# Optimization experiments

Measured on AMD Instinct MI355X. Metric: run time of the kernel, lower is better.

## Reference

```python
import jax, jax.numpy as jnp
import numpy as np

D_MODEL = 1024
NHEAD = 16
HEAD_DIM = D_MODEL // NHEAD
LN_EPS = 1e-5
ROPE_BASE = 10000.0


def _rope_cos_sin(n, head_dim):
    inv_freq = 1.0 / (ROPE_BASE ** (jnp.arange(0, head_dim, 2, dtype=jnp.float32) / head_dim))
    t = jnp.arange(n, dtype=jnp.float32)
    freqs = jnp.outer(t, inv_freq)  # (N, head_dim//2)
    return jnp.cos(freqs), jnp.sin(freqs)


def _apply_rope(x, cos, sin):
    # x: (B, H, N, hd); cos/sin: (N, hd//2)
    B, H, N, hd = x.shape
    xr = x.reshape(B, H, N, hd // 2, 2)
    x0, x1 = xr[..., 0], xr[..., 1]
    c = cos[None, None]
    s = sin[None, None]
    rot = jnp.stack([x0 * c - x1 * s, x0 * s + x1 * c], axis=-1)
    return rot.reshape(B, H, N, hd)


def setup_inputs() -> dict:
    key = jax.random.key(0)
    ks = jax.random.split(key, 6)
    D = D_MODEL
    scale = 1.0 / np.sqrt(D)
    x = jax.random.normal(ks[0], (2, 2048, D), dtype=jnp.float32)
    Wq = jax.random.normal(ks[1], (D, D), dtype=jnp.float32) * scale
    Wk = jax.random.normal(ks[2], (D, D), dtype=jnp.float32) * scale
    Wv = jax.random.normal(ks[3], (D, D), dtype=jnp.float32) * scale
    Wo = jax.random.normal(ks[4], (D, D), dtype=jnp.float32) * scale
    bq = jnp.zeros((D,), jnp.float32)
    bk = jnp.zeros((D,), jnp.float32)
    bv = jnp.zeros((D,), jnp.float32)
    bo = jnp.zeros((D,), jnp.float32)
    ln_w = jnp.ones((D,), jnp.float32)
    ln_b = jnp.zeros((D,), jnp.float32)
    return {"x": x, "ln_w": ln_w, "ln_b": ln_b, "Wq": Wq, "bq": bq,
            "Wk": Wk, "bk": bk, "Wv": Wv, "bv": bv, "Wo": Wo, "bo": bo}


def reference(x, ln_w, ln_b, Wq, bq, Wk, bk, Wv, bv, Wo, bo):
    B, N, D = x.shape
    H, hd = NHEAD, HEAD_DIM
    # LayerNorm
    mu = jnp.mean(x, axis=-1, keepdims=True)
    var = jnp.mean(jnp.square(x - mu), axis=-1, keepdims=True)
    xn = (x - mu) * jax.lax.rsqrt(var + LN_EPS) * ln_w + ln_b
    # QKV projections -> (B, H, N, hd)
    def proj(W, b):
        return (xn @ W.T + b).reshape(B, N, H, hd).transpose(0, 2, 1, 3)
    q = proj(Wq, bq)
    k = proj(Wk, bk)
    v = proj(Wv, bv)
    cos, sin = _rope_cos_sin(N, hd)
    q = _apply_rope(q, cos, sin)
    k = _apply_rope(k, cos, sin)
    scores = jnp.einsum('bhqd,bhkd->bhqk', q, k) / jnp.sqrt(jnp.float32(hd))
    attn = jax.nn.softmax(scores, axis=-1)
    out = jnp.einsum('bhqk,bhkd->bhqd', attn, v)
    out = out.transpose(0, 2, 1, 3).reshape(B, N, D)
    return x + out @ Wo.T + bo
```

## Files before the change

### kernel.cpp

```cpp
#include <hip/hip_runtime.h>


#define SEQ 2048
#define LN_EPS 1e-5f

using short8 = __attribute__((ext_vector_type(8))) short;
using f32x4  = __attribute__((ext_vector_type(4))) float;
using f32x16 = __attribute__((ext_vector_type(16))) float;

__device__ __forceinline__ unsigned short f2bf(float f) {
  union { float f; unsigned u; } v; v.f = f;
  unsigned r = v.u + 0x7FFFu + ((v.u >> 16) & 1u);
  return (unsigned short)(r >> 16);
}

__device__ __forceinline__ void async16(const void* g, void* l) {
  __builtin_amdgcn_global_load_lds(
      (const __attribute__((address_space(1))) void*)g,
      (__attribute__((address_space(3))) void*)l, 16, 0, 0);
}

__global__ __launch_bounds__(256) void prep_kernel(
    const float* __restrict__ x, const float* __restrict__ lnw, const float* __restrict__ lnb,
    const float* __restrict__ wq, const float* __restrict__ wk,
    const float* __restrict__ wv, const float* __restrict__ wo,
    unsigned short* __restrict__ wqkv, unsigned short* __restrict__ wob,
    unsigned short* __restrict__ xn, float2* __restrict__ tab) {
  const int b = blockIdx.x, t = threadIdx.x;
  if (b < 4096) {
    const int gid = b * 256 + t;
    const int m = gid >> 18, e4 = gid & 262143;
    const float* src = (m == 0) ? wq : (m == 1) ? wk : (m == 2) ? wv : wo;
    const float4 v = ((const float4*)src)[e4];
    ushort4 o; o.x = f2bf(v.x); o.y = f2bf(v.y); o.z = f2bf(v.z); o.w = f2bf(v.w);
    if (m < 3) ((ushort4*)wqkv)[(size_t)m * 262144 + e4] = o;
    else       ((ushort4*)wob)[e4] = o;
  } else if (b < 8192) {
    const int row = b - 4096;
    const float4 v = ((const float4*)(x + (size_t)row * 1024))[t];
    float s  = v.x + v.y + v.z + v.w;
    float s2 = v.x * v.x + v.y * v.y + v.z * v.z + v.w * v.w;
#pragma unroll
    for (int off = 32; off >= 1; off >>= 1) {
      s  += __shfl_xor(s, off);
      s2 += __shfl_xor(s2, off);
    }
    __shared__ float red[8];
    const int lane = t & 63, wave = t >> 6;
    if (lane == 0) { red[wave] = s; red[4 + wave] = s2; }
    __syncthreads();
    s  = red[0] + red[1] + red[2] + red[3];
    s2 = red[4] + red[5] + red[6] + red[7];
    const float mu   = s * (1.0f / 1024.0f);
    const float var  = s2 * (1.0f / 1024.0f) - mu * mu;
    const float rstd = rsqrtf(var + LN_EPS);
    const float4 wv4 = ((const float4*)lnw)[t];
    const float4 bv4 = ((const float4*)lnb)[t];
    ushort4 o;
    o.x = f2bf((v.x - mu) * rstd * wv4.x + bv4.x);
    o.y = f2bf((v.y - mu) * rstd * wv4.y + bv4.y);
    o.z = f2bf((v.z - mu) * rstd * wv4.z + bv4.z);
    o.w = f2bf((v.w - mu) * rstd * wv4.w + bv4.w);
    ((ushort4*)xn)[(size_t)row * 256 + t] = o;
  } else {
    const int gid = (b - 8192) * 256 + t;
    const int pos = gid >> 5, ip = gid & 31;
    const float invf = exp2f((float)ip * -0.4152410118609203f);
    const float fr = (float)pos * invf;
    tab[gid] = make_float2(cosf(fr), sinf(fr));
  }
}

__global__ __launch_bounds__(256, 3) void gemm_qkv_kernel(
    const unsigned short* __restrict__ A,
    const unsigned short* __restrict__ Bw,
    const float* __restrict__ bq, const float* __restrict__ bk, const float* __restrict__ bv,
    const float2* __restrict__ tab,
    unsigned short* __restrict__ qb, unsigned short* __restrict__ kbg,
    unsigned short* __restrict__ vtb) {
  __shared__ unsigned short lA[128 * 64];
  __shared__ unsigned short lB[128 * 64];
  const int tid = threadIdx.x;
  const int lane = tid & 63, wave = tid >> 6;
  const int lr = lane & 15, quad = lane >> 4;
  const int wm = (wave >> 1) * 64, wn = (wave & 1) * 64;
  const int n0 = blockIdx.x * 128, m0 = blockIdx.y * 128;
  const int r7 = lr & 7;
  const int lrow = lane >> 3, lcg = (lane & 7) ^ lrow;
  const int lin = blockIdx.y * gridDim.x + blockIdx.x;
  const int phase = ((lin >> 8) * 5) & 15;

  f32x4 acc[4][4];
#pragma unroll
  for (int i = 0; i < 4; ++i)
#pragma unroll
    for (int j = 0; j < 4; ++j) acc[i][j] = (f32x4){0.f, 0.f, 0.f, 0.f};

#define QKV_STAGE(kt_) {                                                        \
    const int kofs = (((kt_) + phase) & 15) * 64;                               \
    _Pragma("unroll")                                                           \
    for (int c = 0; c < 4; ++c) {                                               \
      const int chunk = wave * 4 + c;                                           \
      const int grow = chunk * 8 + lrow;                                        \
      async16(&A[(size_t)(m0 + grow) * 1024 + kofs + lcg * 8], &lA[chunk * 512]);\
      async16(&Bw[(size_t)(n0 + grow) * 1024 + kofs + lcg * 8], &lB[chunk * 512]);\
    }                                                                           \
  }

  QKV_STAGE(0);
  __syncthreads();

  for (int kt = 0; kt < 16; ++kt) {
    short8 a[2][4], b[2][4];
#pragma unroll
    for (int kk = 0; kk < 2; ++kk) {
#pragma unroll
      for (int i = 0; i < 4; ++i)
        a[kk][i] = *(const short8*)&lA[(wm + i * 16 + lr) * 64 + ((kk * 4 + quad) ^ r7) * 8];
#pragma unroll
      for (int j = 0; j < 4; ++j)
        b[kk][j] = *(const short8*)&lB[(wn + j * 16 + lr) * 64 + ((kk * 4 + quad) ^ r7) * 8];
    }
    __syncthreads();
    if (kt < 15) QKV_STAGE(kt + 1);
#pragma unroll
    for (int kk = 0; kk < 2; ++kk)
#pragma unroll
      for (int i = 0; i < 4; ++i)
#pragma unroll
        for (int j = 0; j < 4; ++j)
          acc[i][j] = __builtin_amdgcn_mfma_f32_16x16x32_bf16(a[kk][i], b[kk][j], acc[i][j], 0, 0, 0);
    __syncthreads();
  }

  const int which = n0 >> 10;
  const float* bias = (which == 0) ? bq : (which == 1) ? bk : bv;
  const float qs = (which == 0) ? 0.18033688011112042f : 1.0f;
#pragma unroll
  for (int i = 0; i < 4; ++i)
#pragma unroll
    for (int j = 0; j < 4; ++j)
#pragma unroll
      for (int r = 0; r < 4; ++r) {
        const int row = m0 + wm + i * 16 + quad * 4 + r;
        const int col = n0 + wn + j * 16 + lr;
        const int c = col & 1023;
        float val = (acc[i][j][r] + bias[c]) * qs;
        const int head = c >> 6, hd_i = c & 63;
        const int b_ = row >> 11, pos = row & 2047;
        if (which < 2) {
          const float partner = __shfl_xor(val, 1);
          const float2 cs = tab[(pos << 5) + (hd_i >> 1)];
          val = val * cs.x + partner * ((lane & 1) ? cs.y : -cs.y);
        }
        if (which == 2) {
          vtb[((size_t)((b_ * 16 + head) * 64 + hd_i)) * SEQ + pos] = f2bf(val);
        } else {
          const size_t didx = ((size_t)((b_ * 16 + head) * SEQ + pos)) * 64 + hd_i;
          if (which == 0) qb[didx] = f2bf(val);
          else            kbg[didx] = f2bf(val);
        }
      }
}

__global__ __launch_bounds__(256, 4) void gemm_o_kernel(
    const unsigned short* __restrict__ A,
    const unsigned short* __restrict__ Bw,
    const float* __restrict__ bo, const float* __restrict__ xres, float* __restrict__ out) {
  __shared__ unsigned short lA[64 * 64];
  __shared__ unsigned short lB[64 * 64];
  const int tid = threadIdx.x;
  const int lane = tid & 63, wave = tid >> 6;
  const int lr = lane & 15, quad = lane >> 4;
  const int wm = (wave >> 1) * 32, wn = (wave & 1) * 32;
  const int n0 = blockIdx.x * 64, m0 = blockIdx.y * 64;
  const int r7 = lr & 7;
  const int lrow = lane >> 3, lcg = (lane & 7) ^ lrow;
  const int lin = blockIdx.y * gridDim.x + blockIdx.x;
  const int phase = ((lin >> 8) * 4) & 15;

  f32x4 acc[2][2];
#pragma unroll
  for (int i = 0; i < 2; ++i)
#pragma unroll
    for (int j = 0; j < 2; ++j) acc[i][j] = (f32x4){0.f, 0.f, 0.f, 0.f};

#define O_STAGE(kt_) {                                                          \
    const int kofs = (((kt_) + phase) & 15) * 64;                               \
    _Pragma("unroll")                                                           \
    for (int c = 0; c < 2; ++c) {                                               \
      const int chunk = wave * 2 + c;                                           \
      const int grow = chunk * 8 + lrow;                                        \
      async16(&A[(size_t)(m0 + grow) * 1024 + kofs + lcg * 8], &lA[chunk * 512]);\
      async16(&Bw[(size_t)(n0 + grow) * 1024 + kofs + lcg * 8], &lB[chunk * 512]);\
    }                                                                           \
  }

  O_STAGE(0);
  __syncthreads();

  for (int kt = 0; kt < 16; ++kt) {
    short8 a[2][2], b[2][2];
#pragma unroll
    for (int kk = 0; kk < 2; ++kk) {
#pragma unroll
      for (int i = 0; i < 2; ++i)
        a[kk][i] = *(const short8*)&lA[(wm + i * 16 + lr) * 64 + ((kk * 4 + quad) ^ r7) * 8];
#pragma unroll
      for (int j = 0; j < 2; ++j)
        b[kk][j] = *(const short8*)&lB[(wn + j * 16 + lr) * 64 + ((kk * 4 + quad) ^ r7) * 8];
    }
    __syncthreads();
    if (kt < 15) O_STAGE(kt + 1);
#pragma unroll
    for (int kk = 0; kk < 2; ++kk)
#pragma unroll
      for (int i = 0; i < 2; ++i)
#pragma unroll
        for (int j = 0; j < 2; ++j)
          acc[i][j] = __builtin_amdgcn_mfma_f32_16x16x32_bf16(a[kk][i], b[kk][j], acc[i][j], 0, 0, 0);
    __syncthreads();
  }

#pragma unroll
  for (int i = 0; i < 2; ++i)
#pragma unroll
    for (int j = 0; j < 2; ++j)
#pragma unroll
      for (int r = 0; r < 4; ++r) {
        const int row = m0 + wm + i * 16 + quad * 4 + r;
        const int col = n0 + wn + j * 16 + lr;
        const size_t idx = (size_t)row * 1024 + col;
        out[idx] = acc[i][j][r] + bo[col] + xres[idx];
      }
}

__global__ __launch_bounds__(512, 4) void attn_kernel(
    const unsigned short* __restrict__ qg, const unsigned short* __restrict__ kg,
    const unsigned short* __restrict__ vtg, unsigned short* __restrict__ ao) {
  __shared__ unsigned short lds[32768];
  const int tid = threadIdx.x;
  const int lane = tid & 63, w = tid >> 6;
  const int ws = w & 3, kh = w >> 2;
  const int l31 = lane & 31, hb = lane >> 5;
  const int bh = blockIdx.x >> 4, qt = blockIdx.x & 15;
  const int q0w = qt * 128 + ws * 32;
  const int phase32 = ((blockIdx.x >> 8) & 1) * 16;
  const unsigned short* Q  = qg + (size_t)bh * SEQ * 64;
  const unsigned short* K  = kg + (size_t)bh * SEQ * 64;
  const unsigned short* VT = vtg + (size_t)bh * 64 * SEQ;

  short8 qf[4];
#pragma unroll
  for (int c = 0; c < 4; ++c)
    qf[c] = *(const short8*)&Q[(size_t)(q0w + l31) * 64 + c * 16 + hb * 8];

  f32x16 o[2];
#pragma unroll
  for (int dh = 0; dh < 2; ++dh)
#pragma unroll
    for (int r = 0; r < 16; ++r) o[dh][r] = 0.f;
  float ls = 0.f;

  const int khbase = kh * 1024;
  const int srow_k = ws * 8 + (lane >> 3), gk = lane & 7;
  const int srow_v = ws * 16 + (lane >> 2), gv = lane & 3;
  const unsigned short* Ksrc = K + (size_t)(khbase + srow_k) * 64 + gk * 8;
  const unsigned short* Vsrc = VT + (size_t)srow_v * SEQ + khbase + gv * 8;
  const int kds = (gk * 32 + (srow_k ^ gk)) * 8;
  const int g2s = gv * 2 + (srow_v >> 5);
  const int vds = (g2s * 32 + ((srow_v & 31) ^ g2s)) * 8;
  unsigned short* const base_kh = lds + kh * 4096;

  int koff[4], voff[2][2];
#pragma unroll
  for (int c = 0; c < 4; ++c) {
    const int fk = c * 2 + hb;
    koff[c] = (fk * 32 + (l31 ^ fk)) * 8;
  }
#pragma unroll
  for (int cl = 0; cl < 2; ++cl)
#pragma unroll
    for (int dh = 0; dh < 2; ++dh) {
      const int f = (cl * 2 + hb) * 2 + dh;
      voff[cl][dh] = 2048 + (f * 32 + (l31 ^ f)) * 8;
    }

  auto TILE = [&](const unsigned short* Tb) {
    f32x16 sv;
#pragma unroll
    for (int r = 0; r < 16; ++r) sv[r] = 0.f;
    __builtin_amdgcn_s_setprio(1);
#pragma unroll
    for (int c = 0; c < 4; ++c) {
      const short8 af = *(const short8*)&Tb[koff[c]];
      sv = __builtin_amdgcn_mfma_f32_32x32x16_bf16(af, qf[c], sv, 0, 0, 0);
    }
    __builtin_amdgcn_s_setprio(0);
    unsigned wp[8];
#pragma unroll
    for (int p = 0; p < 8; ++p) {
      union { float f; unsigned u; } e0, e1;
      e0.f = __builtin_amdgcn_exp2f(sv[2 * p]);
      e1.f = __builtin_amdgcn_exp2f(sv[2 * p + 1]);
      ls += e0.f + e1.f;
      wp[p] = __builtin_amdgcn_perm(e1.u, e0.u, 0x07060302u);
    }
    unsigned wlo[8], whi[8];
#pragma unroll
    for (int p = 0; p < 8; ++p) {
      auto rr = __builtin_amdgcn_permlane32_swap(wp[p], wp[p], false, false);
      wlo[p] = rr[0]; whi[p] = rr[1];
    }
    __builtin_amdgcn_s_setprio(1);
#pragma unroll
    for (int cl = 0; cl < 2; ++cl) {
      const int pb = cl * 4;
      union { unsigned u[4]; short8 s; } pf;
      pf.u[0] = hb ? wlo[pb + 2] : wlo[pb + 0];
      pf.u[1] = hb ? wlo[pb + 3] : wlo[pb + 1];
      pf.u[2] = hb ? whi[pb + 2] : whi[pb + 0];
      pf.u[3] = hb ? whi[pb + 3] : whi[pb + 1];
#pragma unroll
      for (int dh = 0; dh < 2; ++dh) {
        const short8 vf = *(const short8*)&Tb[voff[cl][dh]];
        o[dh] = __builtin_amdgcn_mfma_f32_32x32x16_bf16(pf.s, vf, o[dh], 0, 0, 0);
      }
    }
    __builtin_amdgcn_s_setprio(0);
  };

#pragma unroll
  for (int j = 0; j < 2; ++j) {
    const int tl = (j + phase32) & 31;
    const short8 R0 = *(const short8*)(Ksrc + (size_t)tl * 2048);
    const short8 R2 = *(const short8*)(Vsrc + tl * 32);
    *(short8*)(base_kh + j * 8192 + kds) = R0;
    *(short8*)(base_kh + j * 8192 + 2048 + vds) = R2;
  }
  __syncthreads();

  for (int it = 0; it < 16; ++it) {
    const int cs = (it & 1) * 2;
    const int ss = cs ^ 2;
    short8 R0, R2;
    if (it < 15) {
      const int tl = (2 * it + 2 + phase32) & 31;
      R0 = *(const short8*)(Ksrc + (size_t)tl * 2048);
      R2 = *(const short8*)(Vsrc + tl * 32);
    }
    TILE(base_kh + cs * 8192);
    if (it < 15) {
      *(short8*)(base_kh + ss * 8192 + kds) = R0;
      *(short8*)(base_kh + ss * 8192 + 2048 + vds) = R2;
      const int tl = (2 * it + 3 + phase32) & 31;
      R0 = *(const short8*)(Ksrc + (size_t)tl * 2048);
      R2 = *(const short8*)(Vsrc + tl * 32);
    }
    TILE(base_kh + (cs + 1) * 8192);
    if (it < 15) {
      *(short8*)(base_kh + (ss + 1) * 8192 + kds) = R0;
      *(short8*)(base_kh + (ss + 1) * 8192 + 2048 + vds) = R2;
    }
    __syncthreads();
  }

  union { float f; unsigned u; } lsu; lsu.f = ls;
  auto lr2 = __builtin_amdgcn_permlane32_swap(lsu.u, lsu.u, false, false);
  union { unsigned u; float f; } la, lb2; la.u = lr2[0]; lb2.u = lr2[1];
  const float lsH = la.f + lb2.f;

  float* osh = (float*)lds;
  float* lsh = (float*)(lds + 16384);
  if (kh == 1) {
#pragma unroll
    for (int dh = 0; dh < 2; ++dh)
#pragma unroll
      for (int r = 0; r < 16; ++r)
        osh[((ws * 2 + dh) * 16 + r) * 64 + lane] = o[dh][r];
    lsh[ws * 64 + lane] = lsH;
  }
  __syncthreads();
  if (kh == 0) {
    const float rl = 1.0f / (lsH + lsh[ws * 64 + lane]);
    const int b_ = bh >> 4, h = bh & 15;
#pragma unroll
    for (int r = 0; r < 16; ++r) {
      const int m = (r & 3) + 8 * (r >> 2) + 4 * hb;
      const float rlv = __shfl(rl, m);
      const int row = q0w + m;
#pragma unroll
      for (int dh = 0; dh < 2; ++dh) {
        const float ov = o[dh][r] + osh[((ws * 2 + dh) * 16 + r) * 64 + lane];
        ao[(size_t)(b_ * SEQ + row) * 1024 + h * 64 + dh * 32 + l31] = f2bf(ov * rlv);
      }
    }
  }
}

extern "C" void kernel_launch(void* const* d_in, const int* in_sizes, int n_in,
                              void* d_out, int out_size, void* d_ws, size_t ws_size,
                              hipStream_t stream) {
  const float* x   = (const float*)d_in[0];
  const float* lnw = (const float*)d_in[1];
  const float* lnb = (const float*)d_in[2];
  const float* Wq  = (const float*)d_in[3];
  const float* bq  = (const float*)d_in[4];
  const float* Wk  = (const float*)d_in[5];
  const float* bk  = (const float*)d_in[6];
  const float* Wv  = (const float*)d_in[7];
  const float* bv  = (const float*)d_in[8];
  const float* Wo  = (const float*)d_in[9];
  const float* bo  = (const float*)d_in[10];
  float* out = (float*)d_out;

  char* ws = (char*)d_ws;
  unsigned short* wqkv = (unsigned short*)(ws);
  unsigned short* wob  = (unsigned short*)(ws + 6291456);
  unsigned short* xn   = (unsigned short*)(ws + 8388608);
  unsigned short* qb   = (unsigned short*)(ws + 16777216);
  unsigned short* kbuf = (unsigned short*)(ws + 25165824);
  unsigned short* vtb  = (unsigned short*)(ws + 33554432);
  unsigned short* ao   = (unsigned short*)(ws + 41943040);
  float2*         tab  = (float2*)(ws + 50331648);

  hipLaunchKernelGGL(prep_kernel, dim3(8448), dim3(256), 0, stream,
                     x, lnw, lnb, Wq, Wk, Wv, Wo, wqkv, wob, xn, tab);
  hipLaunchKernelGGL(gemm_qkv_kernel, dim3(24, 32), dim3(256), 0, stream,
                     xn, wqkv, bq, bk, bv, tab, qb, kbuf, vtb);
  hipLaunchKernelGGL(attn_kernel, dim3(512), dim3(512), 0, stream, qb, kbuf, vtb, ao);
  hipLaunchKernelGGL(gemm_o_kernel, dim3(16, 64), dim3(256), 0, stream,
                     ao, wob, bo, x, out);
}
```

Baseline: 208.0 us.

## Double-buffer QKV GEMM LDS tiles and remap blocks for XCD-aware locality

Result: slower. 229.2 us (+10.2%).

```diff
diff --git a/kernel.cpp b/kernel.cpp
--- a/kernel.cpp
+++ b/kernel.cpp
@@ -71,23 +71,26 @@
   }
 }
 
-__global__ __launch_bounds__(256, 3) void gemm_qkv_kernel(
+__global__ __launch_bounds__(256, 2) void gemm_qkv_kernel(
     const unsigned short* __restrict__ A,
     const unsigned short* __restrict__ Bw,
     const float* __restrict__ bq, const float* __restrict__ bk, const float* __restrict__ bv,
     const float2* __restrict__ tab,
     unsigned short* __restrict__ qb, unsigned short* __restrict__ kbg,
     unsigned short* __restrict__ vtb) {
-  __shared__ unsigned short lA[128 * 64];
-  __shared__ unsigned short lB[128 * 64];
+  __shared__ unsigned short lA[2][128 * 64];
+  __shared__ unsigned short lB[2][128 * 64];
   const int tid = threadIdx.x;
   const int lane = tid & 63, wave = tid >> 6;
   const int lr = lane & 15, quad = lane >> 4;
   const int wm = (wave >> 1) * 64, wn = (wave & 1) * 64;
-  const int n0 = blockIdx.x * 128, m0 = blockIdx.y * 128;
+  const int lin = blockIdx.x;
+  const int rg = lin & 7, q = lin >> 3;
+  const int bx = (rg & 1) * 12 + q % 12;
+  const int by = (rg >> 1) * 8 + q / 12;
+  const int n0 = bx * 128, m0 = by * 128;
   const int r7 = lr & 7;
   const int lrow = lane >> 3, lcg = (lane & 7) ^ lrow;
-  const int lin = blockIdx.y * gridDim.x + blockIdx.x;
   const int phase = ((lin >> 8) * 5) & 15;
 
   f32x4 acc[4][4];
@@ -96,33 +99,40 @@
 #pragma unroll
     for (int j = 0; j < 4; ++j) acc[i][j] = (f32x4){0.f, 0.f, 0.f, 0.f};
 
-#define QKV_STAGE(kt_) {                                                        \
+#define QKV_STAGE(kt_, LA_, LB_) {                                              \
     const int kofs = (((kt_) + phase) & 15) * 64;                               \
     _Pragma("unroll")                                                           \
     for (int c = 0; c < 4; ++c) {                                               \
       const int chunk = wave * 4 + c;                                           \
       const int grow = chunk * 8 + lrow;                                        \
-      async16(&A[(size_t)(m0 + grow) * 1024 + kofs + lcg * 8], &lA[chunk * 512]);\
-      async16(&Bw[(size_t)(n0 + grow) * 1024 + kofs + lcg * 8], &lB[chunk * 512]);\
+      async16(&A[(size_t)(m0 + grow) * 1024 + kofs + lcg * 8], &(LA_)[chunk * 512]); \
+      async16(&Bw[(size_t)(n0 + grow) * 1024 + kofs + lcg * 8], &(LB_)[chunk * 512]); \
     }                                                                           \
   }
 
-  QKV_STAGE(0);
-  __syncthreads();
+  QKV_STAGE(0, lA[0], lB[0]);
+  QKV_STAGE(1, lA[1], lB[1]);
+  asm volatile("s_waitcnt vmcnt(8)" ::: "memory");
+  __builtin_amdgcn_sched_barrier(0);
+  __builtin_amdgcn_s_barrier();
 
   for (int kt = 0; kt < 16; ++kt) {
+    const int cur = kt & 1;
     short8 a[2][4], b[2][4];
 #pragma unroll
     for (int kk = 0; kk < 2; ++kk) {
 #pragma unroll
       for (int i = 0; i < 4; ++i)
-        a[kk][i] = *(const short8*)&lA[(wm + i * 16 + lr) * 64 + ((kk * 4 + quad) ^ r7) * 8];
+        a[kk][i] = *(const short8*)&lA[cur][(wm + i * 16 + lr) * 64 + ((kk * 4 + quad) ^ r7) * 8];
 #pragma unroll
       for (int j = 0; j < 4; ++j)
-        b[kk][j] = *(const short8*)&lB[(wn + j * 16 + lr) * 64 + ((kk * 4 + quad) ^ r7) * 8];
-    }
-    __syncthreads();
-    if (kt < 15) QKV_STAGE(kt + 1);
+        b[kk][j] = *(const short8*)&lB[cur][(wn + j * 16 + lr) * 64 + ((kk * 4 + quad) ^ r7) * 8];
+    }
+    asm volatile("s_waitcnt lgkmcnt(0)" ::: "memory");
+    __builtin_amdgcn_sched_barrier(0);
+    __builtin_amdgcn_s_barrier();
+    __builtin_amdgcn_sched_barrier(0);
+    if (kt < 14) QKV_STAGE(kt + 2, lA[cur], lB[cur]);
 #pragma unroll
     for (int kk = 0; kk < 2; ++kk)
 #pragma unroll
@@ -130,7 +140,13 @@
 #pragma unroll
         for (int j = 0; j < 4; ++j)
           acc[i][j] = __builtin_amdgcn_mfma_f32_16x16x32_bf16(a[kk][i], b[kk][j], acc[i][j], 0, 0, 0);
-    __syncthreads();
+    if (kt < 15) {
+      if (kt < 14) asm volatile("s_waitcnt vmcnt(8)" ::: "memory");
+      else         asm volatile("s_waitcnt vmcnt(0)" ::: "memory");
+      __builtin_amdgcn_sched_barrier(0);
+      __builtin_amdgcn_s_barrier();
+      __builtin_amdgcn_sched_barrier(0);
+    }
   }
 
   const int which = n0 >> 10;
@@ -173,10 +189,13 @@
   const int lane = tid & 63, wave = tid >> 6;
   const int lr = lane & 15, quad = lane >> 4;
   const int wm = (wave >> 1) * 32, wn = (wave & 1) * 32;
-  const int n0 = blockIdx.x * 64, m0 = blockIdx.y * 64;
+  const int lin = blockIdx.x;
+  const int rg = lin & 7, q = lin >> 3;
+  const int bx = q % 16;
+  const int by = rg * 8 + q / 16;
+  const int n0 = bx * 64, m0 = by * 64;
   const int r7 = lr & 7;
   const int lrow = lane >> 3, lcg = (lane & 7) ^ lrow;
-  const int lin = blockIdx.y * gridDim.x + blockIdx.x;
   const int phase = ((lin >> 8) * 4) & 15;
 
   f32x4 acc[2][2];
@@ -426,9 +445,9 @@
 
   hipLaunchKernelGGL(prep_kernel, dim3(8448), dim3(256), 0, stream,
                      x, lnw, lnb, Wq, Wk, Wv, Wo, wqkv, wob, xn, tab);
-  hipLaunchKernelGGL(gemm_qkv_kernel, dim3(24, 32), dim3(256), 0, stream,
+  hipLaunchKernelGGL(gemm_qkv_kernel, dim3(768), dim3(256), 0, stream,
                      xn, wqkv, bq, bk, bv, tab, qb, kbuf, vtb);
   hipLaunchKernelGGL(attn_kernel, dim3(512), dim3(512), 0, stream, qb, kbuf, vtb, ao);
-  hipLaunchKernelGGL(gemm_o_kernel, dim3(16, 64), dim3(256), 0, stream,
+  hipLaunchKernelGGL(gemm_o_kernel, dim3(1024), dim3(256), 0, stream,
                      ao, wob, bo, x, out);
 }
```

## Remap QKV GEMM grid to grouped tile order and simplify O-proj load loop

Applied to the files above, without the earlier changes.

Result: slower. 213.4 us (+2.6%).

```diff
diff --git a/kernel.cpp b/kernel.cpp
--- a/kernel.cpp
+++ b/kernel.cpp
@@ -84,10 +84,13 @@
   const int lane = tid & 63, wave = tid >> 6;
   const int lr = lane & 15, quad = lane >> 4;
   const int wm = (wave >> 1) * 64, wn = (wave & 1) * 64;
-  const int n0 = blockIdx.x * 128, m0 = blockIdx.y * 128;
+  const int lin = blockIdx.x;
+  const int rg = lin & 7, q = lin >> 3;
+  const int bx = (rg & 1) * 12 + q % 12;
+  const int by = (rg >> 1) * 8 + q / 12;
+  const int n0 = bx * 128, m0 = by * 128;
   const int r7 = lr & 7;
   const int lrow = lane >> 3, lcg = (lane & 7) ^ lrow;
-  const int lin = blockIdx.y * gridDim.x + blockIdx.x;
   const int phase = ((lin >> 8) * 5) & 15;
 
   f32x4 acc[4][4];
@@ -185,41 +188,32 @@
 #pragma unroll
     for (int j = 0; j < 2; ++j) acc[i][j] = (f32x4){0.f, 0.f, 0.f, 0.f};
 
-#define O_STAGE(kt_) {                                                          \
-    const int kofs = (((kt_) + phase) & 15) * 64;                               \
-    _Pragma("unroll")                                                           \
-    for (int c = 0; c < 2; ++c) {                                               \
-      const int chunk = wave * 2 + c;                                           \
-      const int grow = chunk * 8 + lrow;                                        \
-      async16(&A[(size_t)(m0 + grow) * 1024 + kofs + lcg * 8], &lA[chunk * 512]);\
-      async16(&Bw[(size_t)(n0 + grow) * 1024 + kofs + lcg * 8], &lB[chunk * 512]);\
-    }                                                                           \
-  }
-
-  O_STAGE(0);
-  __syncthreads();
-
   for (int kt = 0; kt < 16; ++kt) {
-    short8 a[2][2], b[2][2];
+    const int kofs = ((kt + phase) & 15) * 64;
+    __syncthreads();
+#pragma unroll
+    for (int c = 0; c < 2; ++c) {
+      const int chunk = wave * 2 + c;
+      const int grow = chunk * 8 + lrow;
+      async16(&A[(size_t)(m0 + grow) * 1024 + kofs + lcg * 8], &lA[chunk * 512]);
+      async16(&Bw[(size_t)(n0 + grow) * 1024 + kofs + lcg * 8], &lB[chunk * 512]);
+    }
+    __syncthreads();
 #pragma unroll
     for (int kk = 0; kk < 2; ++kk) {
+      short8 a[2], b[2];
 #pragma unroll
       for (int i = 0; i < 2; ++i)
-        a[kk][i] = *(const short8*)&lA[(wm + i * 16 + lr) * 64 + ((kk * 4 + quad) ^ r7) * 8];
+        a[i] = *(const short8*)&lA[(wm + i * 16 + lr) * 64 + ((kk * 4 + quad) ^ r7) * 8];
 #pragma unroll
       for (int j = 0; j < 2; ++j)
-        b[kk][j] = *(const short8*)&lB[(wn + j * 16 + lr) * 64 + ((kk * 4 + quad) ^ r7) * 8];
-    }
-    __syncthreads();
-    if (kt < 15) O_STAGE(kt + 1);
-#pragma unroll
-    for (int kk = 0; kk < 2; ++kk)
+        b[j] = *(const short8*)&lB[(wn + j * 16 + lr) * 64 + ((kk * 4 + quad) ^ r7) * 8];
 #pragma unroll
       for (int i = 0; i < 2; ++i)
 #pragma unroll
         for (int j = 0; j < 2; ++j)
-          acc[i][j] = __builtin_amdgcn_mfma_f32_16x16x32_bf16(a[kk][i], b[kk][j], acc[i][j], 0, 0, 0);
-    __syncthreads();
+          acc[i][j] = __builtin_amdgcn_mfma_f32_16x16x32_bf16(a[i], b[j], acc[i][j], 0, 0, 0);
+    }
   }
 
 #pragma unroll
@@ -426,7 +420,7 @@
 
   hipLaunchKernelGGL(prep_kernel, dim3(8448), dim3(256), 0, stream,
                      x, lnw, lnb, Wq, Wk, Wv, Wo, wqkv, wob, xn, tab);
-  hipLaunchKernelGGL(gemm_qkv_kernel, dim3(24, 32), dim3(256), 0, stream,
+  hipLaunchKernelGGL(gemm_qkv_kernel, dim3(768), dim3(256), 0, stream,
                      xn, wqkv, bq, bk, bv, tab, qb, kbuf, vtb);
   hipLaunchKernelGGL(attn_kernel, dim3(512), dim3(512), 0, stream, qb, kbuf, vtb, ao);
   hipLaunchKernelGGL(gemm_o_kernel, dim3(16, 64), dim3(256), 0, stream,
```
